# Kernel optimization log

Hardware: AMD Instinct MI355X
Metric: run time of the kernel (lower is better)

## Reference

```python
import jax, jax.numpy as jnp
import numpy as np

D_MODEL = 1024
HEADS = 16
HEAD_DIM = D_MODEL // HEADS
FF = 4 * D_MODEL
EPS = 1e-5


def _layer_norm(x, g, b):
    mu = jnp.mean(x, axis=-1, keepdims=True)
    var = jnp.mean(jnp.square(x - mu), axis=-1, keepdims=True)
    return (x - mu) * jax.lax.rsqrt(var + EPS) * g + b


def setup_inputs() -> dict:
    key = jax.random.key(0)
    ks = jax.random.split(key, 12)
    s = 0.02
    inp = {
        "x": jax.random.normal(ks[0], (2, 2048, D_MODEL), dtype=jnp.float32),
        "Wq": jax.random.normal(ks[1], (D_MODEL, D_MODEL), dtype=jnp.float32) * s,
        "bq": jnp.zeros((D_MODEL,), jnp.float32),
        "Wk": jax.random.normal(ks[2], (D_MODEL, D_MODEL), dtype=jnp.float32) * s,
        "bk": jnp.zeros((D_MODEL,), jnp.float32),
        "Wv": jax.random.normal(ks[3], (D_MODEL, D_MODEL), dtype=jnp.float32) * s,
        "bv": jnp.zeros((D_MODEL,), jnp.float32),
        "Wm": jax.random.normal(ks[4], (D_MODEL, D_MODEL), dtype=jnp.float32) * s,
        "bm": jnp.zeros((D_MODEL,), jnp.float32),
        "W1": jax.random.normal(ks[5], (D_MODEL, FF), dtype=jnp.float32) * s,
        "b1": jnp.zeros((FF,), jnp.float32),
        "W2": jax.random.normal(ks[6], (FF, D_MODEL), dtype=jnp.float32) * s,
        "b2": jnp.zeros((D_MODEL,), jnp.float32),
        "g1": jnp.ones((D_MODEL,), jnp.float32),
        "be1": jnp.zeros((D_MODEL,), jnp.float32),
        "g2": jnp.ones((D_MODEL,), jnp.float32),
        "be2": jnp.zeros((D_MODEL,), jnp.float32),
    }
    return inp


def reference(x, Wq, bq, Wk, bk, Wv, bv, Wm, bm, W1, b1, W2, b2, g1, be1, g2, be2):
    B, L, _ = x.shape
    # self-attention: source = x, no pos, no masks
    q = (x @ Wq + bq).reshape(B, L, HEADS, HEAD_DIM).transpose(0, 2, 1, 3)
    k = (x @ Wk + bk).reshape(B, L, HEADS, HEAD_DIM).transpose(0, 2, 1, 3)
    v = (x @ Wv + bv).reshape(B, L, HEADS, HEAD_DIM).transpose(0, 2, 1, 3)
    scale = 1.0 / np.sqrt(HEAD_DIM).astype(np.float32)
    scores = jnp.einsum("bhld,bhsd->bhls", q, k) * scale  # [B,H,L,L]
    attn = jax.nn.softmax(scores, axis=-1)
    msg = jnp.einsum("bhls,bhsd->bhld", attn, v)
    msg = msg.transpose(0, 2, 1, 3).reshape(B, L, D_MODEL)
    msg = msg @ Wm + bm
    h = _layer_norm(x + msg, g1, be1)
    ffn = jax.nn.relu(h @ W1 + b1) @ W2 + b2
    return _layer_norm(h + ffn, g2, be2)
```

## Files before the change

### kernel.cpp

```cpp
#include <hip/hip_runtime.h>

#define D_MODEL 1024
#define N_TOK   4096
#define HEADS   16
#define FF_DIM  4096
#define SEQ_L   2048

typedef unsigned short u16;
typedef unsigned int   u32;
typedef __bf16 bf16x8 __attribute__((ext_vector_type(8)));
typedef float  f32x4  __attribute__((ext_vector_type(4)));

#define AS1C(p) ((const __attribute__((address_space(1))) void*)(p))
#define AS3(p)  ((__attribute__((address_space(3))) void*)(p))

__device__ __forceinline__ u16 f2bf(float f) {
    union { float f; unsigned u; } c; c.f = f;
    return (u16)((c.u + 0x7fffu + ((c.u >> 16) & 1u)) >> 16);
}
__device__ __forceinline__ float bf2f(u16 b) {
    union { unsigned u; float f; } c; c.u = ((unsigned)b) << 16;
    return c.f;
}
__device__ __forceinline__ u32 cvt_pk_bf16(float lo, float hi) {
    u32 r;
    asm("v_cvt_pk_bf16_f32 %0, %1, %2" : "=v"(r) : "v"(lo), "v"(hi));
    return r;
}
__device__ __forceinline__ float fmax3(float a, float b, float c) {
    float r;
    asm("v_max3_f32 %0, %1, %2, %3" : "=v"(r) : "v"(a), "v"(b), "v"(c));
    return r;
}

template<int RELU>
__global__ __launch_bounds__(512, 2)
void gemm_pipe(const u16* __restrict__ A, const u16* __restrict__ Bt,
               const float* __restrict__ bias, u16* __restrict__ C,
               int M, int N, int K)
{
    __shared__ u16 As[2][256 * 64];
    __shared__ u16 Bs[2][256 * 64];

    const int tid = threadIdx.x;
    const int wid = tid >> 6, lane = tid & 63;
    const int wr  = wid >> 2, wc = wid & 3;
    const int l15 = lane & 15, l16 = lane >> 4;

    const int nwg = gridDim.x * gridDim.y;
    int bid = blockIdx.y * gridDim.x + blockIdx.x;
    bid = (bid & 7) * (nwg >> 3) + (bid >> 3);
    const int r0 = (bid / gridDim.x) * 256, c0 = (bid % gridDim.x) * 256;

    const u16* Ab = A  + (size_t)r0 * K;
    const u16* Bb = Bt + (size_t)c0 * K;

    f32x4 acc[8][4];
#pragma unroll
    for (int m = 0; m < 8; ++m)
#pragma unroll
        for (int n = 0; n < 4; ++n) acc[m][n] = (f32x4){0.f, 0.f, 0.f, 0.f};

    auto stage = [&](u16* dst, const u16* src, int kbase) {
#pragma unroll
        for (int i = 0; i < 4; ++i) {
            const int r  = i * 64 + (tid >> 3);
            const int gc = (tid & 7) ^ (r & 7);
            __builtin_amdgcn_global_load_lds(AS1C(src + (size_t)r * K + kbase + gc * 8),
                                             AS3(dst + (i * 64 + (wid << 3)) * 64), 16, 0, 0);
        }
    };

    bf16x8 af[4][2], bbA[2][2], bbB[2][2];

    auto ldAf = [&](const u16* sl, int mh) {
#pragma unroll
        for (int m = 0; m < 4; ++m) {
            const int row = wr * 128 + (mh * 4 + m) * 16 + l15;
#pragma unroll
            for (int ks = 0; ks < 2; ++ks) {
                const int ch = (ks * 4 + l16) ^ (row & 7);
                af[m][ks] = *(const bf16x8*)&sl[row * 64 + ch * 8];
            }
        }
    };
    auto ldBf = [&](const u16* sl, int pair, bf16x8 (&bb)[2][2]) {
#pragma unroll
        for (int n = 0; n < 2; ++n) {
            const int row = wc * 64 + (pair * 2 + n) * 16 + l15;
#pragma unroll
            for (int ks = 0; ks < 2; ++ks) {
                const int ch = (ks * 4 + l16) ^ (row & 7);
                bb[n][ks] = *(const bf16x8*)&sl[row * 64 + ch * 8];
            }
        }
    };
    auto mm16 = [&](int mh, int pair, bf16x8 (&bb)[2][2]) {
        __builtin_amdgcn_s_setprio(1);
#pragma unroll
        for (int ks = 0; ks < 2; ++ks)
#pragma unroll
            for (int m = 0; m < 4; ++m)
#pragma unroll
                for (int n = 0; n < 2; ++n)
                    acc[mh * 4 + m][pair * 2 + n] =
                        __builtin_amdgcn_mfma_f32_16x16x32_bf16(af[m][ks], bb[n][ks],
                                                                acc[mh * 4 + m][pair * 2 + n], 0, 0, 0);
        __builtin_amdgcn_s_setprio(0);
    };

    const int nt = K >> 6;
    stage(&As[0][0], Ab, 0);
    stage(&Bs[0][0], Bb, 0);
    stage(&As[1][0], Ab, 64);

    for (int t = 0; t < nt; ++t) {
        u16* Asl = &As[t & 1][0];
        u16* Bsl = &Bs[t & 1][0];
        u16* Aso = &As[t & 1][0];
        u16* Bso = &Bs[(t + 1) & 1][0];

        if (t + 1 < nt) { asm volatile("s_waitcnt vmcnt(4)" ::: "memory"); }
        else            { asm volatile("s_waitcnt vmcnt(0)" ::: "memory"); }
        __builtin_amdgcn_s_barrier();
        ldAf(Asl, 0);
        ldBf(Bsl, 0, bbA);
        if (t + 1 < nt) stage(Bso, Bb, (t + 1) * 64);
        __builtin_amdgcn_s_barrier();
        mm16(0, 0, bbA);
        __builtin_amdgcn_s_barrier();
        ldBf(Bsl, 1, bbB);
        mm16(0, 1, bbB);
        __builtin_amdgcn_s_barrier();
        ldAf(Asl, 1);
        mm16(1, 0, bbA);
        __builtin_amdgcn_s_barrier();
        if (t + 2 < nt) stage(Aso, Ab, (t + 2) * 64);
        mm16(1, 1, bbB);
        __builtin_amdgcn_s_barrier();
    }

#pragma unroll
    for (int n = 0; n < 4; ++n) {
        const int col = c0 + wc * 64 + n * 16 + l15;
        const float bv = bias[col];
#pragma unroll
        for (int m = 0; m < 8; ++m) {
#pragma unroll
            for (int r = 0; r < 4; ++r) {
                const size_t row = (size_t)(r0 + wr * 128 + m * 16 + l16 * 4 + r);
                float v = acc[m][n][r] + bv;
                if (RELU) v = fmaxf(v, 0.f);
                C[row * N + col] = f2bf(v);
            }
        }
    }
}

template<int RELU>
__global__ __launch_bounds__(512, 2)
void gemm_pipe128(const u16* __restrict__ A, const u16* __restrict__ Bt,
                  const float* __restrict__ bias, u16* __restrict__ C,
                  int M, int N, int K)
{
    __shared__ u16 As[2][128 * 64];
    __shared__ u16 Bs[2][128 * 64];

    const int tid = threadIdx.x;
    const int wid = tid >> 6, lane = tid & 63;
    const int wr  = wid >> 2, wc = wid & 3;
    const int l15 = lane & 15, l16 = lane >> 4;

    const int nwg = gridDim.x * gridDim.y;
    int bid = blockIdx.y * gridDim.x + blockIdx.x;
    bid = (bid & 7) * (nwg >> 3) + (bid >> 3);
    const int r0 = (bid / gridDim.x) * 128, c0 = (bid % gridDim.x) * 128;

    const u16* Ab = A  + (size_t)r0 * K;
    const u16* Bb = Bt + (size_t)c0 * K;

    f32x4 acc[4][2];
#pragma unroll
    for (int m = 0; m < 4; ++m)
#pragma unroll
        for (int n = 0; n < 2; ++n) acc[m][n] = (f32x4){0.f, 0.f, 0.f, 0.f};

    auto stage = [&](u16* dst, const u16* src, int kbase) {
#pragma unroll
        for (int i = 0; i < 2; ++i) {
            const int r  = i * 64 + (tid >> 3);
            const int gc = (tid & 7) ^ (r & 7);
            __builtin_amdgcn_global_load_lds(AS1C(src + (size_t)r * K + kbase + gc * 8),
                                             AS3(dst + (i * 64 + (wid << 3)) * 64), 16, 0, 0);
        }
    };

    const int nt = K >> 6;
    stage(&As[0][0], Ab, 0);  stage(&Bs[0][0], Bb, 0);
    stage(&As[1][0], Ab, 64); stage(&Bs[1][0], Bb, 64);

    for (int t = 0; t < nt; ++t) {
        const u16* Asl = &As[t & 1][0];
        const u16* Bsl = &Bs[t & 1][0];

        if (t + 1 < nt) { asm volatile("s_waitcnt vmcnt(4)" ::: "memory"); }
        else            { asm volatile("s_waitcnt vmcnt(0)" ::: "memory"); }
        __builtin_amdgcn_s_barrier();

        bf16x8 af[4][2], bb[2][2];
#pragma unroll
        for (int m = 0; m < 4; ++m) {
            const int row = wr * 64 + m * 16 + l15;
#pragma unroll
            for (int ks = 0; ks < 2; ++ks) {
                const int ch = (ks * 4 + l16) ^ (row & 7);
                af[m][ks] = *(const bf16x8*)&Asl[row * 64 + ch * 8];
            }
        }
#pragma unroll
        for (int n = 0; n < 2; ++n) {
            const int row = wc * 32 + n * 16 + l15;
#pragma unroll
            for (int ks = 0; ks < 2; ++ks) {
                const int ch = (ks * 4 + l16) ^ (row & 7);
                bb[n][ks] = *(const bf16x8*)&Bsl[row * 64 + ch * 8];
            }
        }
        __builtin_amdgcn_s_setprio(1);
#pragma unroll
        for (int ks = 0; ks < 2; ++ks)
#pragma unroll
            for (int m = 0; m < 4; ++m)
#pragma unroll
                for (int n = 0; n < 2; ++n)
                    acc[m][n] = __builtin_amdgcn_mfma_f32_16x16x32_bf16(af[m][ks], bb[n][ks], acc[m][n], 0, 0, 0);
        __builtin_amdgcn_s_setprio(0);
        __builtin_amdgcn_s_barrier();

        if (t + 2 < nt) {
            stage(&As[t & 1][0], Ab, (t + 2) * 64);
            stage(&Bs[t & 1][0], Bb, (t + 2) * 64);
        }
    }

#pragma unroll
    for (int n = 0; n < 2; ++n) {
        const int col = c0 + wc * 32 + n * 16 + l15;
        const float bv = bias[col];
#pragma unroll
        for (int m = 0; m < 4; ++m) {
#pragma unroll
            for (int r = 0; r < 4; ++r) {
                const size_t row = (size_t)(r0 + wr * 64 + m * 16 + l16 * 4 + r);
                float v = acc[m][n][r] + bv;
                if (RELU) v = fmaxf(v, 0.f);
                C[row * N + col] = f2bf(v);
            }
        }
    }
}

__global__ __launch_bounds__(512, 4)
void attn_mfma(const u16* __restrict__ qkv, u16* __restrict__ ao)
{
    __shared__ u16 Kl[2][128 * 64];
    __shared__ u32 Vt[64 * 64];

    const int tid = threadIdx.x;
    const int wid = tid >> 6, lane = tid & 63;
    const int l15 = lane & 15, l16 = lane >> 4;

    int lin = blockIdx.y * gridDim.x + blockIdx.x;
    lin = (lin & 7) * 64 + (lin >> 3);
    const int bh = lin >> 4, b = bh >> 4, h = bh & 15;
    const int q0 = (lin & 15) * 128;
    const int ho = h * 64;
    const size_t tb = (size_t)b * SEQ_L;

    const u16* qg = qkv + (tb + q0) * 3072 + ho;
    const u16* kg = qkv + tb * 3072 + 1024 + ho;
    const u16* vg = qkv + tb * 3072 + 2048 + ho;

    const float SC = 0.18033688f;

    bf16x8 qa[2];
#pragma unroll
    for (int ks = 0; ks < 2; ++ks) {
        union { bf16x8 v; u16 u[8]; u32 w[4]; } a, r;
        a.v = *(const bf16x8*)(qg + (size_t)(wid * 16 + l15) * 3072 + ks * 32 + l16 * 8);
#pragma unroll
        for (int e = 0; e < 4; ++e)
            r.w[e] = cvt_pk_bf16(bf2f(a.u[2 * e]) * SC, bf2f(a.u[2 * e + 1]) * SC);
        qa[ks] = r.v;
    }

    const int sp = lane;
    const int dc = wid;

    auto stageK = [&](int buf, int s0) {
#pragma unroll
        for (int i = 0; i < 2; ++i) {
            const int r  = i * 64 + (tid >> 3);
            const int gc = (tid & 7) ^ (r & 7);
            __builtin_amdgcn_global_load_lds(AS1C(kg + (size_t)(s0 + r) * 3072 + gc * 8),
                                             AS3(&Kl[buf][(i * 64 + wid * 8) * 64]), 16, 0, 0);
        }
    };

    f32x4 oacc[4];
#pragma unroll
    for (int f = 0; f < 4; ++f) oacc[f] = (f32x4){0.f, 0.f, 0.f, 0.f};
    float m_c = -1e30f, l_c = 0.f;

    union { bf16x8 v; u16 u[8]; } ua, ub;
    stageK(0, 0);
    ua.v = *(const bf16x8*)(vg + (size_t)(2 * sp) * 3072 + dc * 8);
    ub.v = *(const bf16x8*)(vg + (size_t)(2 * sp + 1) * 3072 + dc * 8);

    const int nt = SEQ_L / 128;
    for (int t = 0; t < nt; ++t) {
        const int buf = t & 1;

        asm volatile("s_waitcnt vmcnt(0)" ::: "memory");
#pragma unroll
        for (int e = 0; e < 8; ++e) {
            const int d = dc * 8 + e;
            const int w = sp ^ (((d & 7) << 2) ^ ((d >> 3) << 1));
            Vt[d * 64 + w] = (u32)ua.u[e] | ((u32)ub.u[e] << 16);
        }
        __syncthreads();

        if (t + 1 < nt) {
            stageK(buf ^ 1, (t + 1) * 128);
            ua.v = *(const bf16x8*)(vg + (size_t)((t + 1) * 128 + 2 * sp) * 3072 + dc * 8);
            ub.v = *(const bf16x8*)(vg + (size_t)((t + 1) * 128 + 2 * sp + 1) * 3072 + dc * 8);
        }

        f32x4 sacc[8];
#pragma unroll
        for (int f = 0; f < 8; ++f) sacc[f] = (f32x4){0.f, 0.f, 0.f, 0.f};
#pragma unroll
        for (int ks = 0; ks < 2; ++ks)
#pragma unroll
            for (int f = 0; f < 8; ++f) {
                const int row = f * 16 + l15;
                const int ch  = (ks * 4 + l16) ^ (row & 7);
                bf16x8 kb = *(const bf16x8*)&Kl[buf][row * 64 + ch * 8];
                sacc[f] = __builtin_amdgcn_mfma_f32_16x16x32_bf16(kb, qa[ks], sacc[f], 0, 0, 0);
            }

        float pm[8];
#pragma unroll
        for (int f = 0; f < 8; ++f)
            pm[f] = fmaxf(fmax3(sacc[f][0], sacc[f][1], sacc[f][2]), sacc[f][3]);
        float mx;
        {
            float t0 = fmax3(pm[0], pm[1], pm[2]);
            float t1 = fmax3(pm[3], pm[4], pm[5]);
            float t2 = fmaxf(pm[6], pm[7]);
            mx = fmax3(t0, t1, t2);
        }
        mx = fmaxf(mx, __shfl_xor(mx, 16));
        mx = fmaxf(mx, __shfl_xor(mx, 32));

        if (__any(mx > m_c + 8.f)) {
            const float mnew = fmaxf(m_c, mx);
            const float corr = __builtin_exp2f(m_c - mnew);
            m_c = mnew;
            l_c *= corr;
#pragma unroll
            for (int r = 0; r < 4; ++r) {
                const float cr = __shfl(corr, l16 * 4 + r);
#pragma unroll
                for (int f = 0; f < 4; ++f) oacc[f][r] *= cr;
            }
        }

        float rs = 0.f;
#pragma unroll
        for (int f = 0; f < 8; ++f)
#pragma unroll
            for (int r = 0; r < 4; ++r) {
                const float p = __builtin_exp2f(sacc[f][r] - m_c);
                sacc[f][r] = p; rs += p;
            }
        rs += __shfl_xor(rs, 16);
        rs += __shfl_xor(rs, 32);
        l_c += rs;

        u32 pk[8][2];
#pragma unroll
        for (int f = 0; f < 8; ++f) {
            pk[f][0] = cvt_pk_bf16(sacc[f][0], sacc[f][1]);
            pk[f][1] = cvt_pk_bf16(sacc[f][2], sacc[f][3]);
        }

#pragma unroll
        for (int S = 0; S < 4; ++S) {
            union { bf16x8 v; u32 u[4]; } af;
            af.u[0] = pk[2 * S][0];     af.u[1] = pk[2 * S][1];
            af.u[2] = pk[2 * S + 1][0]; af.u[3] = pk[2 * S + 1][1];
#pragma unroll
            for (int f2 = 0; f2 < 4; ++f2) {
                const int d = f2 * 16 + l15;
                const int swzd = ((d & 7) << 2) ^ ((d >> 3) << 1);
                union { bf16x8 v; uint2 u[2]; } vb;
                vb.u[0] = *(const uint2*)&Vt[d * 64 + ((16 * S + 2 * l16) ^ swzd)];
                vb.u[1] = *(const uint2*)&Vt[d * 64 + ((16 * S + 8 + 2 * l16) ^ swzd)];
                oacc[f2] = __builtin_amdgcn_mfma_f32_16x16x32_bf16(af.v, vb.v, oacc[f2], 0, 0, 0);
            }
        }
        __syncthreads();
    }

#pragma unroll
    for (int r = 0; r < 4; ++r) {
        const float ld  = __shfl(l_c, l16 * 4 + r);
        const float inv = 1.f / ld;
        const size_t row = tb + q0 + wid * 16 + l16 * 4 + r;
#pragma unroll
        for (int f2 = 0; f2 < 4; ++f2)
            ao[row * 1024 + ho + f2 * 16 + l15] = f2bf(oacc[f2][r] * inv);
    }
}

template<int WB>
__global__ __launch_bounds__(256)
void add_ln(const float* __restrict__ x, const u16* __restrict__ y,
            const float* __restrict__ g, const float* __restrict__ be,
            float* __restrict__ outf, u16* __restrict__ outb)
{
    __shared__ float red[4];
    const int t = blockIdx.x, tid = threadIdx.x;
    const int c = tid * 4, lane = tid & 63, wv = tid >> 6;

    float4 a = *(const float4*)(x + (size_t)t * D_MODEL + c);
    ushort4 yb = *(const ushort4*)(y + (size_t)t * D_MODEL + c);
    float s[4] = {a.x + bf2f(yb.x), a.y + bf2f(yb.y), a.z + bf2f(yb.z), a.w + bf2f(yb.w)};

    float ps = s[0] + s[1] + s[2] + s[3];
#pragma unroll
    for (int off = 32; off > 0; off >>= 1) ps += __shfl_down(ps, off);
    if (lane == 0) red[wv] = ps;
    __syncthreads();
    const float mean = (red[0] + red[1] + red[2] + red[3]) * (1.f / D_MODEL);
    __syncthreads();

    float pv = 0.f;
#pragma unroll
    for (int u = 0; u < 4; ++u) { float d = s[u] - mean; pv += d * d; }
#pragma unroll
    for (int off = 32; off > 0; off >>= 1) pv += __shfl_down(pv, off);
    if (lane == 0) red[wv] = pv;
    __syncthreads();
    const float var = (red[0] + red[1] + red[2] + red[3]) * (1.f / D_MODEL);
    const float inv = rsqrtf(var + 1e-5f);

    float4 g4 = *(const float4*)(g + c);
    float4 b4 = *(const float4*)(be + c);
    float o[4];
#pragma unroll
    for (int u = 0; u < 4; ++u) o[u] = (s[u] - mean) * inv;
    float4 of = {o[0] * g4.x + b4.x, o[1] * g4.y + b4.y, o[2] * g4.z + b4.z, o[3] * g4.w + b4.w};
    *(float4*)(outf + (size_t)t * D_MODEL + c) = of;
    if (WB) {
        ushort4 ob = {f2bf(of.x), f2bf(of.y), f2bf(of.z), f2bf(of.w)};
        *(ushort4*)(outb + (size_t)t * D_MODEL + c) = ob;
    }
}

__global__ __launch_bounds__(256)
void prep(const float* __restrict__ Wq, const float* __restrict__ Wk,
          const float* __restrict__ Wv, const float* __restrict__ Wm,
          const float* __restrict__ W1, const float* __restrict__ W2,
          const float* __restrict__ x,
          const float* __restrict__ bq, const float* __restrict__ bk,
          const float* __restrict__ bv,
          u16* __restrict__ wqkv_t, u16* __restrict__ wm_t,
          u16* __restrict__ w1_t, u16* __restrict__ w2_t,
          u16* __restrict__ xb, float* __restrict__ bqkv)
{
    const int blk = blockIdx.x, tid = threadIdx.x;
    if (blk < 3072) {
        __shared__ float T[64][65];
        const float* src; u16* dst; int K, N, tile;
        if (blk < 256)       { src = Wq; dst = wqkv_t;               K = 1024; N = 1024; tile = blk; }
        else if (blk < 512)  { src = Wk; dst = wqkv_t + 1024 * 1024; K = 1024; N = 1024; tile = blk - 256; }
        else if (blk < 768)  { src = Wv; dst = wqkv_t + 2*1024*1024; K = 1024; N = 1024; tile = blk - 512; }
        else if (blk < 1024) { src = Wm; dst = wm_t;                 K = 1024; N = 1024; tile = blk - 768; }
        else if (blk < 2048) { src = W1; dst = w1_t;                 K = 1024; N = 4096; tile = blk - 1024; }
        else                 { src = W2; dst = w2_t;                 K = 4096; N = 1024; tile = blk - 2048; }
        const int ntn = N >> 6;
        const int n0 = (tile % ntn) * 64, k0 = (tile / ntn) * 64;
        const int rr = tid >> 4, cc = (tid & 15) * 4;
#pragma unroll
        for (int u = 0; u < 4; ++u) {
            const float4 v = *(const float4*)(src + (size_t)(k0 + rr + u * 16) * N + n0 + cc);
            T[rr + u * 16][cc + 0] = v.x; T[rr + u * 16][cc + 1] = v.y;
            T[rr + u * 16][cc + 2] = v.z; T[rr + u * 16][cc + 3] = v.w;
        }
        __syncthreads();
#pragma unroll
        for (int u = 0; u < 4; ++u) {
            const int n = rr + u * 16;
            ushort4 o;
            o.x = f2bf(T[cc + 0][n]); o.y = f2bf(T[cc + 1][n]);
            o.z = f2bf(T[cc + 2][n]); o.w = f2bf(T[cc + 3][n]);
            *(ushort4*)(dst + (size_t)(n0 + n) * K + k0 + cc) = o;
        }
    } else if (blk < 3072 + 4096) {
        const int i = (blk - 3072) * 1024 + tid * 4;
        float4 v = *(const float4*)(x + i);
        ushort4 o = {f2bf(v.x), f2bf(v.y), f2bf(v.z), f2bf(v.w)};
        *(ushort4*)(xb + i) = o;
    } else {
#pragma unroll
        for (int u = 0; u < 12; ++u) {
            const int i = u * 256 + tid;
            bqkv[i] = i < 1024 ? bq[i] : (i < 2048 ? bk[i - 1024] : bv[i - 2048]);
        }
    }
}

extern "C" void kernel_launch(void* const* d_in, const int* in_sizes, int n_in,
                              void* d_out, int out_size, void* d_ws, size_t ws_size,
                              hipStream_t stream)
{
    (void)in_sizes; (void)n_in; (void)out_size; (void)ws_size;

    const float* x   = (const float*)d_in[0];
    const float* Wq  = (const float*)d_in[1];
    const float* bq  = (const float*)d_in[2];
    const float* Wk  = (const float*)d_in[3];
    const float* bk  = (const float*)d_in[4];
    const float* Wv  = (const float*)d_in[5];
    const float* bv  = (const float*)d_in[6];
    const float* Wm  = (const float*)d_in[7];
    const float* bm  = (const float*)d_in[8];
    const float* W1  = (const float*)d_in[9];
    const float* b1  = (const float*)d_in[10];
    const float* W2  = (const float*)d_in[11];
    const float* b2  = (const float*)d_in[12];
    const float* g1  = (const float*)d_in[13];
    const float* be1 = (const float*)d_in[14];
    const float* g2  = (const float*)d_in[15];
    const float* be2 = (const float*)d_in[16];
    float* out = (float*)d_out;

    char* base = (char*)d_ws;
    const size_t MB = 1u << 20;
    u16*   wqkv_t = (u16*)(base);
    u16*   wm_t   = (u16*)(base + 6 * MB);
    u16*   w1_t   = (u16*)(base + 8 * MB);
    u16*   w2_t   = (u16*)(base + 16 * MB);
    float* bqkv   = (float*)(base + 24 * MB);
    u16*   xb     = (u16*)(base + 25 * MB);
    u16*   qkv    = (u16*)(base + 33 * MB);
    u16*   ao     = (u16*)(base + 57 * MB);
    u16*   f1     = (u16*)(base + 33 * MB);
    u16*   msg    = (u16*)(base + 25 * MB);
    u16*   ffn    = (u16*)(base + 25 * MB);
    float* hf     = (float*)(base + 65 * MB);
    u16*   hb     = (u16*)(base + 81 * MB);

    dim3 blk(256);
    prep<<<dim3(3072 + 4096 + 1), blk, 0, stream>>>(Wq, Wk, Wv, Wm, W1, W2, x,
                                                    bq, bk, bv,
                                                    wqkv_t, wm_t, w1_t, w2_t, xb, bqkv);

    gemm_pipe<0><<<dim3(12, 16), dim3(512), 0, stream>>>(xb, wqkv_t, bqkv, qkv, N_TOK, 3072, 1024);
    attn_mfma<<<dim3(SEQ_L / 128, 32), dim3(512), 0, stream>>>(qkv, ao);
    gemm_pipe128<0><<<dim3(8, 32), dim3(512), 0, stream>>>(ao, wm_t, bm, msg, N_TOK, 1024, 1024);
    add_ln<1><<<dim3(N_TOK), blk, 0, stream>>>(x, msg, g1, be1, hf, hb);
    gemm_pipe<1><<<dim3(16, 16), dim3(512), 0, stream>>>(hb, w1_t, b1, f1, N_TOK, FF_DIM, 1024);
    gemm_pipe128<0><<<dim3(8, 32), dim3(512), 0, stream>>>(f1, w2_t, b2, ffn, N_TOK, 1024, FF_DIM);
    add_ln<0><<<dim3(N_TOK), blk, 0, stream>>>(hf, ffn, g2, be2, out, nullptr);
}
```

Baseline: 256.2 us.

## Use 256-thread 128x128 GEMM for QKV/out/FFN2 and MFMA row-sum in attention

The 128x128 GEMM kernel now uses 4 waves instead of 8, with each wave computing a 64x64 sub-tile (4x4 MFMA fragments), which raises register reuse per wave. This kernel replaces the 256x256 gemm_pipe for the QKV projection (grid 24x32). In attention, the softmax row sum is no longer a VALU reduction with cross-lane shuffles; it is accumulated by an extra MFMA against a vector of bf16 ones. The trade-offs are more accumulator registers per thread and a row sum taken from the bf16-rounded probabilities, which changes numerics slightly.

```diff
diff --git a/kernel.cpp b/kernel.cpp
--- a/kernel.cpp
+++ b/kernel.cpp
@@ -158,8 +158,8 @@
 }
 
 template<int RELU>
-__global__ __launch_bounds__(512, 2)
-void gemm_pipe128(const u16* __restrict__ A, const u16* __restrict__ Bt,
+__global__ __launch_bounds__(256, 2)
+void gemm_tile128(const u16* __restrict__ A, const u16* __restrict__ Bt,
                   const float* __restrict__ bias, u16* __restrict__ C,
                   int M, int N, int K)
 {
@@ -168,7 +168,7 @@
 
     const int tid = threadIdx.x;
     const int wid = tid >> 6, lane = tid & 63;
-    const int wr  = wid >> 2, wc = wid & 3;
+    const int wr  = wid >> 1, wc = wid & 1;
     const int l15 = lane & 15, l16 = lane >> 4;
 
     const int nwg = gridDim.x * gridDim.y;
@@ -179,19 +179,19 @@
     const u16* Ab = A  + (size_t)r0 * K;
     const u16* Bb = Bt + (size_t)c0 * K;
 
-    f32x4 acc[4][2];
+    f32x4 acc[4][4];
 #pragma unroll
     for (int m = 0; m < 4; ++m)
 #pragma unroll
-        for (int n = 0; n < 2; ++n) acc[m][n] = (f32x4){0.f, 0.f, 0.f, 0.f};
+        for (int n = 0; n < 4; ++n) acc[m][n] = (f32x4){0.f, 0.f, 0.f, 0.f};
 
     auto stage = [&](u16* dst, const u16* src, int kbase) {
 #pragma unroll
-        for (int i = 0; i < 2; ++i) {
-            const int r  = i * 64 + (tid >> 3);
+        for (int i = 0; i < 4; ++i) {
+            const int r  = i * 32 + (tid >> 3);
             const int gc = (tid & 7) ^ (r & 7);
             __builtin_amdgcn_global_load_lds(AS1C(src + (size_t)r * K + kbase + gc * 8),
-                                             AS3(dst + (i * 64 + (wid << 3)) * 64), 16, 0, 0);
+                                             AS3(dst + (i * 32 + (wid << 3)) * 64), 16, 0, 0);
         }
     };
 
@@ -203,11 +203,11 @@
         const u16* Asl = &As[t & 1][0];
         const u16* Bsl = &Bs[t & 1][0];
 
-        if (t + 1 < nt) { asm volatile("s_waitcnt vmcnt(4)" ::: "memory"); }
+        if (t + 1 < nt) { asm volatile("s_waitcnt vmcnt(8)" ::: "memory"); }
         else            { asm volatile("s_waitcnt vmcnt(0)" ::: "memory"); }
         __builtin_amdgcn_s_barrier();
 
-        bf16x8 af[4][2], bb[2][2];
+        bf16x8 af[4][2], bb[4][2];
 #pragma unroll
         for (int m = 0; m < 4; ++m) {
             const int row = wr * 64 + m * 16 + l15;
@@ -218,8 +218,8 @@
             }
         }
 #pragma unroll
-        for (int n = 0; n < 2; ++n) {
-            const int row = wc * 32 + n * 16 + l15;
+        for (int n = 0; n < 4; ++n) {
+            const int row = wc * 64 + n * 16 + l15;
 #pragma unroll
             for (int ks = 0; ks < 2; ++ks) {
                 const int ch = (ks * 4 + l16) ^ (row & 7);
@@ -232,7 +232,7 @@
 #pragma unroll
             for (int m = 0; m < 4; ++m)
 #pragma unroll
-                for (int n = 0; n < 2; ++n)
+                for (int n = 0; n < 4; ++n)
                     acc[m][n] = __builtin_amdgcn_mfma_f32_16x16x32_bf16(af[m][ks], bb[n][ks], acc[m][n], 0, 0, 0);
         __builtin_amdgcn_s_setprio(0);
         __builtin_amdgcn_s_barrier();
@@ -244,8 +244,8 @@
     }
 
 #pragma unroll
-    for (int n = 0; n < 2; ++n) {
-        const int col = c0 + wc * 32 + n * 16 + l15;
+    for (int n = 0; n < 4; ++n) {
+        const int col = c0 + wc * 64 + n * 16 + l15;
         const float bv = bias[col];
 #pragma unroll
         for (int m = 0; m < 4; ++m) {
@@ -294,6 +294,10 @@
         qa[ks] = r.v;
     }
 
+    union { bf16x8 v; u32 u[4]; } onesv;
+#pragma unroll
+    for (int e = 0; e < 4; ++e) onesv.u[e] = 0x3F803F80u;
+
     const int sp = lane;
     const int dc = wid;
 
@@ -310,7 +314,8 @@
     f32x4 oacc[4];
 #pragma unroll
     for (int f = 0; f < 4; ++f) oacc[f] = (f32x4){0.f, 0.f, 0.f, 0.f};
-    float m_c = -1e30f, l_c = 0.f;
+    f32x4 lcol = (f32x4){0.f, 0.f, 0.f, 0.f};
+    float m_c = -1e30f;
 
     union { bf16x8 v; u16 u[8]; } ua, ub;
     stageK(0, 0);
@@ -367,26 +372,20 @@
             const float mnew = fmaxf(m_c, mx);
             const float corr = __builtin_exp2f(m_c - mnew);
             m_c = mnew;
-            l_c *= corr;
 #pragma unroll
             for (int r = 0; r < 4; ++r) {
                 const float cr = __shfl(corr, l16 * 4 + r);
+                lcol[r] *= cr;
 #pragma unroll
                 for (int f = 0; f < 4; ++f) oacc[f][r] *= cr;
             }
         }
 
-        float rs = 0.f;
 #pragma unroll
         for (int f = 0; f < 8; ++f)
 #pragma unroll
-            for (int r = 0; r < 4; ++r) {
-                const float p = __builtin_exp2f(sacc[f][r] - m_c);
-                sacc[f][r] = p; rs += p;
-            }
-        rs += __shfl_xor(rs, 16);
-        rs += __shfl_xor(rs, 32);
-        l_c += rs;
+            for (int r = 0; r < 4; ++r)
+                sacc[f][r] = __builtin_exp2f(sacc[f][r] - m_c);
 
         u32 pk[8][2];
 #pragma unroll
@@ -409,14 +408,14 @@
                 vb.u[1] = *(const uint2*)&Vt[d * 64 + ((16 * S + 8 + 2 * l16) ^ swzd)];
                 oacc[f2] = __builtin_amdgcn_mfma_f32_16x16x32_bf16(af.v, vb.v, oacc[f2], 0, 0, 0);
             }
+            lcol = __builtin_amdgcn_mfma_f32_16x16x32_bf16(af.v, onesv.v, lcol, 0, 0, 0);
         }
         __syncthreads();
     }
 
 #pragma unroll
     for (int r = 0; r < 4; ++r) {
-        const float ld  = __shfl(l_c, l16 * 4 + r);
-        const float inv = 1.f / ld;
+        const float inv = 1.f / lcol[r];
         const size_t row = tb + q0 + wid * 16 + l16 * 4 + r;
 #pragma unroll
         for (int f2 = 0; f2 < 4; ++f2)
@@ -568,11 +567,11 @@
                                                     bq, bk, bv,
                                                     wqkv_t, wm_t, w1_t, w2_t, xb, bqkv);
 
-    gemm_pipe<0><<<dim3(12, 16), dim3(512), 0, stream>>>(xb, wqkv_t, bqkv, qkv, N_TOK, 3072, 1024);
+    gemm_tile128<0><<<dim3(24, 32), blk, 0, stream>>>(xb, wqkv_t, bqkv, qkv, N_TOK, 3072, 1024);
     attn_mfma<<<dim3(SEQ_L / 128, 32), dim3(512), 0, stream>>>(qkv, ao);
-    gemm_pipe128<0><<<dim3(8, 32), dim3(512), 0, stream>>>(ao, wm_t, bm, msg, N_TOK, 1024, 1024);
+    gemm_tile128<0><<<dim3(8, 32), blk, 0, stream>>>(ao, wm_t, bm, msg, N_TOK, 1024, 1024);
     add_ln<1><<<dim3(N_TOK), blk, 0, stream>>>(x, msg, g1, be1, hf, hb);
     gemm_pipe<1><<<dim3(16, 16), dim3(512), 0, stream>>>(hb, w1_t, b1, f1, N_TOK, FF_DIM, 1024);
-    gemm_pipe128<0><<<dim3(8, 32), dim3(512), 0, stream>>>(f1, w2_t, b2, ffn, N_TOK, 1024, FF_DIM);
+    gemm_tile128<0><<<dim3(8, 32), blk, 0, stream>>>(f1, w2_t, b2, ffn, N_TOK, 1024, FF_DIM);
     add_ln<0><<<dim3(N_TOK), blk, 0, stream>>>(hf, ffn, g2, be2, out, nullptr);
 }
```

Result: slower. 267.9 us (+4.6%).
